# Performance work log

Hardware: AMD Instinct MI355X
Metric: run time of the kernel (lower is better)

The kernel has to match this reference:

```python
import jax, jax.numpy as jnp
import numpy as np
import math

INV = 1.0 / (2.0 * math.pi) ** 2  # 1/(2*pi)^2 normalization used throughout
EPS = 1e-8


def setup_inputs() -> dict:
    key = jax.random.key(0)
    ks = jax.random.split(key, 5)
    N, K, J = 512, 8, 6
    return {
        "x_hat": jax.random.normal(ks[0], (N, N, 2), jnp.float32),
        "phi_hat_real": jax.random.normal(ks[1], (N, N), jnp.float32),
        "phi_hat_imag": jax.random.normal(ks[2], (N, N), jnp.float32),
        "psi_hat_real": jax.random.normal(ks[3], (K, J, N, N), jnp.float32),
        "psi_hat_imag": jax.random.normal(ks[4], (K, J, N, N), jnp.float32),
    }


def reference(x_hat, phi_hat_real, phi_hat_imag, psi_hat_real, psi_hat_imag):
    K, J, N, _ = psi_hat_real.shape
    NN = N * N
    phi2 = phi_hat_real ** 2 + phi_hat_imag ** 2  # [N,N]

    # zeroth-order coefficient: full spatial mean of |x_hat|^2 * |phi_hat|^2
    s0 = INV * jnp.mean((x_hat[:, :, 0] ** 2 + x_hat[:, :, 1] ** 2) * phi2)

    # first layer: complex multiply in Fourier domain, ifft2, modulus, fft2
    xc = jax.lax.complex(x_hat[:, :, 0], x_hat[:, :, 1])          # [N,N] complex
    psic = jax.lax.complex(psi_hat_real, psi_hat_imag)            # [K,J,N,N] complex
    temp = jnp.fft.ifft2(xc[None, None] * psic, axes=(-2, -1))    # [K,J,N,N] complex
    mod = jnp.sqrt(temp.real ** 2 + temp.imag ** 2 + EPS)         # modulus nonlinearity
    t2 = jnp.fft.fft2(mod, axes=(-2, -1))                         # rfft onesided=False == full fft of real
    power = (t2.real ** 2 + t2.imag ** 2).reshape(K, J, NN)       # |U1_hat|^2

    # first-order coefficients a[k,i] = INV * mean(power * phi2)
    a = INV * (power @ phi2.reshape(NN)) / NN                     # [K,J]

    # second-order coefficients via GEMM over spatial dim:
    # B[k,i,m,j] = INV * mean_xy(power[k,i] * |psi[m,j]|^2)
    psi2 = (psi_hat_real ** 2 + psi_hat_imag ** 2).reshape(K, J, NN)
    B = INV * jnp.einsum('kin,mjn->kimj', power, psi2) / NN       # [K,J,K,J]

    # assemble output in the same concatenation order as the torch loop:
    # [s0, a_0, b_0(flattened over k,m,j'), a_1, b_1, ..., a_{J-1}]
    pieces = [s0[None]]
    for i in range(J):
        pieces.append(a[:, i])
        if i < J - 1:
            pieces.append(B[:, i, :, i + 1:J].reshape(-1))
    return jnp.concatenate(pieces, axis=0)
```

## Files before the change

kernel.cpp:

```cpp
#include <hip/hip_runtime.h>
#include <hip/hip_fp16.h>

#define Nn 512
#define NNe 262144
#define CST 546

__device__ __forceinline__ float2 f2(float x, float y){ return make_float2(x, y); }
__device__ __forceinline__ float2 cadd(float2 a, float2 b){ return f2(a.x+b.x, a.y+b.y); }
__device__ __forceinline__ float2 csub(float2 a, float2 b){ return f2(a.x-b.x, a.y-b.y); }
__device__ __forceinline__ float2 cmul(float2 a, float2 b){
    return f2(a.x*b.x - a.y*b.y, a.x*b.y + a.y*b.x);
}
__device__ __forceinline__ int pidx(int p){ return p + (p>>4) + (p>>7); }
#define WFENCE() __builtin_amdgcn_wave_barrier()

template<int SGN>
__device__ __forceinline__ void fft8(float2 a[8]){
    const float r = 0.7071067811865476f;
    const float S = (float)SGN;
    float2 u0 = cadd(a[0], a[4]), u1 = cadd(a[1], a[5]);
    float2 u2 = cadd(a[2], a[6]), u3 = cadd(a[3], a[7]);
    float2 v0 = csub(a[0], a[4]), v1 = csub(a[1], a[5]);
    float2 v2 = csub(a[2], a[6]), v3 = csub(a[3], a[7]);
    v1 = cmul(v1, f2(r, S*r));
    v2 = cmul(v2, f2(0.f, S));
    v3 = cmul(v3, f2(-r, S*r));
    float2 p0 = cadd(u0, u2), p1 = cadd(u1, u3);
    float2 q0 = csub(u0, u2), q1 = cmul(csub(u1, u3), f2(0.f, S));
    a[0] = cadd(p0, p1); a[4] = csub(p0, p1);
    a[2] = cadd(q0, q1); a[6] = csub(q0, q1);
    p0 = cadd(v0, v2); p1 = cadd(v1, v3);
    q0 = csub(v0, v2); q1 = cmul(csub(v1, v3), f2(0.f, S));
    a[1] = cadd(p0, p1); a[5] = csub(p0, p1);
    a[3] = cadd(q0, q1); a[7] = csub(q0, q1);
}

__device__ __forceinline__ float2 twdp(int idx, float inv){
    float ang = 6.283185307179586f * (inv * (float)idx);
    float s, c;
    __sincosf(ang, &s, &c);
    return f2(c, s);
}

template<int SGN>
__device__ void fft512_dif_i(float2 v[8], float2* buf, int lane){
    fft8<SGN>(v);
    {
        float2 w1 = twdp(lane, 1.f/512.f);
        if (SGN < 0) w1.y = -w1.y;
        float2 w  = f2(1.f, 0.f);
        #pragma unroll
        for (int r = 0; r < 8; ++r){
            buf[pidx(r*64 + lane)] = cmul(v[r], w);
            w = cmul(w, w1);
        }
    }
    WFENCE();
    int rb = (lane >> 3) * 64, t2 = lane & 7;
    float2 y[8];
    #pragma unroll
    for (int q = 0; q < 8; ++q) y[q] = buf[pidx(rb + t2 + 8*q)];
    fft8<SGN>(y);
    WFENCE();
    {
        float2 w2 = twdp(t2, 1.f/64.f);
        if (SGN < 0) w2.y = -w2.y;
        float2 w  = f2(1.f, 0.f);
        #pragma unroll
        for (int r = 0; r < 8; ++r){
            buf[pidx(rb + r*8 + t2)] = cmul(y[r], w);
            w = cmul(w, w2);
        }
    }
    WFENCE();
    int base = rb + t2*8;
    #pragma unroll
    for (int q = 0; q < 8; ++q) v[q] = buf[pidx(base + q)];
    fft8<SGN>(v);
}

template<int SGN>
__device__ void fft512_dit_i(float2 v[8], float2* buf, int lane){
    int rb = (lane >> 3) * 64, t2 = lane & 7;
    fft8<SGN>(v);
    int base = rb + t2*8;
    #pragma unroll
    for (int q = 0; q < 8; ++q) buf[pidx(base + q)] = v[q];
    WFENCE();
    float2 y[8];
    #pragma unroll
    for (int r = 0; r < 8; ++r) y[r] = buf[pidx(rb + r*8 + t2)];
    {
        float2 w2 = twdp(t2, 1.f/64.f);
        if (SGN < 0) w2.y = -w2.y;
        float2 w  = f2(1.f, 0.f);
        #pragma unroll
        for (int r = 0; r < 8; ++r){
            y[r] = cmul(y[r], w);
            w = cmul(w, w2);
        }
    }
    fft8<SGN>(y);
    WFENCE();
    #pragma unroll
    for (int q = 0; q < 8; ++q) buf[pidx(rb + t2 + 8*q)] = y[q];
    WFENCE();
    #pragma unroll
    for (int r = 0; r < 8; ++r) v[r] = buf[pidx(r*64 + lane)];
    {
        float2 w1 = twdp(lane, 1.f/512.f);
        if (SGN < 0) w1.y = -w1.y;
        float2 w  = f2(1.f, 0.f);
        #pragma unroll
        for (int r = 0; r < 8; ++r){
            v[r] = cmul(v[r], w);
            w = cmul(w, w1);
        }
    }
    fft8<SGN>(v);
}

__global__ __launch_bounds__(256, 6)
void k_mulrow(const float2* __restrict__ xh, const float* __restrict__ pr,
              const float* __restrict__ pi, __half2* __restrict__ temp,
              __half* __restrict__ psi2h){
    __shared__ float2 lds[4][548];
    int wave = threadIdx.x >> 6, lane = threadIdx.x & 63;
    int img  = blockIdx.x >> 7;
    int row  = ((blockIdx.x & 127) << 2) | wave;
    size_t boff = (size_t)img * NNe + (size_t)row * Nn;
    const float2* xr = xh + (size_t)row * Nn;
    float2 v[8];
    #pragma unroll
    for (int q = 0; q < 8; ++q){
        int x = lane + 64*q;
        float2 xv = xr[x];
        float2 pv = f2(pr[boff + x], pi[boff + x]);
        psi2h[boff + x] = __float2half_rn(pv.x*pv.x + pv.y*pv.y);
        v[q] = cmul(xv, pv);
    }
    fft512_dif_i<1>(v, lds[wave], lane);
    __half2* outp = temp + boff;
    #pragma unroll
    for (int q = 0; q < 8; ++q) outp[64*q + lane] = __floats2half2_rn(v[q].x, v[q].y);
}

__global__ __launch_bounds__(512, 2)
void k_colfused(__half2* __restrict__ temp){
    __shared__ __half2 st[16][521];
    __shared__ float2 fbuf[8][CST];
    int img = blockIdx.x >> 5;
    int x0  = (blockIdx.x & 31) << 4;
    __half2* src = temp + (size_t)img * NNe + x0;
    for (int i = threadIdx.x; i < 2048; i += 512){
        int row = i >> 2, c4 = (i & 3) << 2;
        uint4 u = *(const uint4*)&src[(size_t)row * Nn + c4];
        st[c4+0][row] = *(__half2*)&u.x;
        st[c4+1][row] = *(__half2*)&u.y;
        st[c4+2][row] = *(__half2*)&u.z;
        st[c4+3][row] = *(__half2*)&u.w;
    }
    __syncthreads();
    int wave = threadIdx.x >> 6, lane = threadIdx.x & 63;
    const float sc = 3.814697265625e-06f;
    float2* buf = fbuf[wave];
    int c0 = 2*wave, c1 = c0 + 1;
    float2 a[8], b[8];
    #pragma unroll
    for (int q = 0; q < 8; ++q) a[q] = __half22float2(st[c0][lane + 64*q]);
    fft512_dif_i<1>(a, buf, lane);
    WFENCE();
    #pragma unroll
    for (int q = 0; q < 8; ++q) b[q] = __half22float2(st[c1][lane + 64*q]);
    fft512_dif_i<1>(b, buf, lane);
    float2 z[8];
    #pragma unroll
    for (int q = 0; q < 8; ++q){
        float r0 = a[q].x*sc, i0 = a[q].y*sc;
        float r1 = b[q].x*sc, i1 = b[q].y*sc;
        z[q] = f2(sqrtf(r0*r0 + i0*i0 + 1e-8f), sqrtf(r1*r1 + i1*i1 + 1e-8f));
    }
    WFENCE();
    fft512_dit_i<-1>(z, buf, lane);
    #pragma unroll
    for (int q = 0; q < 8; ++q) buf[pidx(lane + 64*q)] = z[q];
    WFENCE();
    #pragma unroll
    for (int q = 0; q < 8; ++q){
        int k = lane + 64*q;
        float2 zr = buf[pidx((512 - k) & 511)];
        float2 zv = z[q];
        st[c0][k] = __floats2half2_rn(0.5f*(zv.x + zr.x), 0.5f*(zv.y - zr.y));
        st[c1][k] = __floats2half2_rn(0.5f*(zv.y + zr.y), 0.5f*(zr.x - zv.x));
    }
    __syncthreads();
    for (int i = threadIdx.x; i < 2048; i += 512){
        int row = i >> 2, c4 = (i & 3) << 2;
        uint4 u;
        *(__half2*)&u.x = st[c4+0][row];
        *(__half2*)&u.y = st[c4+1][row];
        *(__half2*)&u.z = st[c4+2][row];
        *(__half2*)&u.w = st[c4+3][row];
        *(uint4*)&src[(size_t)row * Nn + c4] = u;
    }
}

__global__ __launch_bounds__(256, 6)
void k_rowpow(const __half2* __restrict__ temp, __half* __restrict__ powerh){
    __shared__ float2 lds[4][548];
    int wave = threadIdx.x >> 6, lane = threadIdx.x & 63;
    int img  = blockIdx.x >> 7;
    int row  = ((blockIdx.x & 127) << 2) | wave;
    const __half2* src = temp + (size_t)img * NNe + (size_t)row * Nn;
    float2 v[8];
    #pragma unroll
    for (int q = 0; q < 8; ++q) v[q] = __half22float2(src[64*q + lane]);
    fft512_dit_i<-1>(v, lds[wave], lane);
    __half* dst = powerh + (size_t)img * NNe + (size_t)row * Nn;
    #pragma unroll
    for (int q = 0; q < 8; ++q)
        dst[lane + 64*q] = __float2half_rn((v[q].x*v[q].x + v[q].y*v[q].y) * 0.00390625f);
}

__global__ __launch_bounds__(128)
void k_gemm(const __half* __restrict__ powerh, const __half* __restrict__ psi2h,
            const float* __restrict__ phr, const float* __restrict__ phii,
            const float2* __restrict__ xh, float* __restrict__ partC,
            float* __restrict__ partS0){
    __shared__ __align__(16) float P[2][48][68];
    __shared__ __align__(16) float W[2][56][68];
    int wave = threadIdx.x >> 6, lane = threadIdx.x & 63;
    float (*Pw)[68] = P[wave];
    float (*Ww)[68] = W[wave];
    int gw = blockIdx.x*2 + wave;
    int lm = lane >> 3, lw = lane & 7;
    float acc[6][7] = {};
    float s0acc = 0.f;
    #pragma unroll
    for (int r = 49; r < 56; ++r){
        Ww[r][lane] = 0.f;
        if (lane < 4) Ww[r][64 + lane] = 0.f;
    }
    int n0 = gw * 256;
    for (int st = 0; st < 4; ++st){
        int nb = n0 + st*64;
        WFENCE();
        #pragma unroll
        for (int rr = 0; rr < 12; ++rr){
            int row = rr*4 + (lane >> 4);
            int c4  = (lane & 15) * 4;
            size_t off = (size_t)row*NNe + nb + c4;
            const __half2* p2 = (const __half2*)&powerh[off];
            float2 f0 = __half22float2(p2[0]);
            float2 f1 = __half22float2(p2[1]);
            *(float4*)&Pw[row][c4] = make_float4(f0.x, f0.y, f1.x, f1.y);
        }
        #pragma unroll
        for (int rr = 0; rr < 12; ++rr){
            int row = rr*4 + (lane >> 4);
            int c4  = (lane & 15) * 4;
            size_t off = (size_t)row*NNe + nb + c4;
            const __half2* p2 = (const __half2*)&psi2h[off];
            float2 f0 = __half22float2(p2[0]);
            float2 f1 = __half22float2(p2[1]);
            *(float4*)&Ww[row][c4] = make_float4(f0.x, f0.y, f1.x, f1.y);
        }
        if (lane < 16){
            int c4 = lane * 4;
            float4 a = *(const float4*)&phr[nb + c4];
            float4 b = *(const float4*)&phii[nb + c4];
            float4 w4;
            w4.x = a.x*a.x + b.x*b.x; w4.y = a.y*a.y + b.y*b.y;
            w4.z = a.z*a.z + b.z*b.z; w4.w = a.w*a.w + b.w*b.w;
            *(float4*)&Ww[48][c4] = w4;
        }
        WFENCE();
        {
            float2 xv = xh[nb + lane];
            s0acc = fmaf(xv.x*xv.x + xv.y*xv.y, Ww[48][lane], s0acc);
        }
        #pragma unroll 2
        for (int nn = 0; nn < 64; nn += 4){
            float4 pa[6], wb[7];
            #pragma unroll
            for (int i = 0; i < 6; ++i) pa[i] = *(const float4*)&Pw[lm + 8*i][nn];
            #pragma unroll
            for (int j = 0; j < 7; ++j) wb[j] = *(const float4*)&Ww[lw + 8*j][nn];
            #pragma unroll
            for (int i = 0; i < 6; ++i)
                #pragma unroll
                for (int j = 0; j < 7; ++j){
                    float s = acc[i][j];
                    s = fmaf(pa[i].x, wb[j].x, s);
                    s = fmaf(pa[i].y, wb[j].y, s);
                    s = fmaf(pa[i].z, wb[j].z, s);
                    s = fmaf(pa[i].w, wb[j].w, s);
                    acc[i][j] = s;
                }
        }
    }
    #pragma unroll
    for (int o = 32; o > 0; o >>= 1) s0acc += __shfl_down(s0acc, o, 64);
    if (lane == 0) partS0[gw] = s0acc;
    float* outp = partC + (size_t)gw * 2400;
    #pragma unroll
    for (int i = 0; i < 6; ++i)
        #pragma unroll
        for (int j = 0; j < 7; ++j){
            int m = lm + 8*i, wc = lw + 8*j;
            if (wc < 49) outp[m*50 + wc] = acc[i][j];
        }
}

__global__ __launch_bounds__(256)
void k_redc1(const float* __restrict__ partC, float* __restrict__ partC2){
    __shared__ float red[4][64];
    int es = threadIdx.x & 63, wave = threadIdx.x >> 6;
    int e = blockIdx.x*64 + es;
    int b0 = blockIdx.y*64 + wave*16;
    float s = 0.f;
    if (e < 2400){
        #pragma unroll
        for (int u = 0; u < 16; ++u) s += partC[(size_t)(b0+u)*2400 + e];
    }
    red[wave][es] = s;
    __syncthreads();
    if (wave == 0 && e < 2400)
        partC2[(size_t)blockIdx.y*2400 + e] = red[0][es]+red[1][es]+red[2][es]+red[3][es];
}

__global__ __launch_bounds__(256)
void k_final(const float* __restrict__ partC2, const float* __restrict__ partS0,
             float* __restrict__ outp, float SC0, float SCC){
    __shared__ float CFs[2400];
    __shared__ float ssum[4];
    int tid = threadIdx.x, wave = tid >> 6, lane = tid & 63;
    for (int e = tid; e < 2400; e += 256){
        float s = 0.f;
        #pragma unroll
        for (int u = 0; u < 16; ++u) s += partC2[(size_t)u*2400 + e];
        CFs[e] = SCC * s;
    }
    float a = 0.f;
    #pragma unroll
    for (int u = 0; u < 4; ++u) a += partS0[tid + 256*u];
    #pragma unroll
    for (int o = 32; o > 0; o >>= 1) a += __shfl_down(a, o, 64);
    if (lane == 0) ssum[wave] = a;
    __syncthreads();
    if (tid == 0) outp[0] = SC0 * (ssum[0]+ssum[1]+ssum[2]+ssum[3]);
    int off = 1;
    for (int i = 0; i < 6; ++i){
        if (tid < 8) outp[off + tid] = CFs[(tid*6 + i)*50 + 48];
        off += 8;
        if (i < 5){
            int nj = 5 - i, cnt = 64 * nj;
            for (int p = tid; p < cnt; p += 256){
                int j2 = p % nj;
                int km = p / nj;
                int m = km & 7, k = km >> 3;
                outp[off + p] = CFs[(k*6 + i)*50 + m*6 + (i + 1 + j2)];
            }
            off += cnt;
        }
    }
}

extern "C" void kernel_launch(void* const* d_in, const int* in_sizes, int n_in,
                              void* d_out, int out_size, void* d_ws, size_t ws_size,
                              hipStream_t stream){
    (void)in_sizes; (void)n_in; (void)out_size; (void)ws_size;
    const float2* xh  = (const float2*)d_in[0];
    const float*  phr = (const float*)d_in[1];
    const float*  phi_= (const float*)d_in[2];
    const float*  psr = (const float*)d_in[3];
    const float*  psi_= (const float*)d_in[4];
    float* outp = (float*)d_out;
    float* ws   = (float*)d_ws;

    size_t o_power = 0;
    size_t o_partC = o_power + (size_t)24 * NNe;
    size_t o_pC2   = o_partC + (size_t)1024 * 2400;
    size_t o_s0    = o_pC2 + (size_t)16 * 2400;
    size_t o_temp  = o_s0 + 1024;
    size_t o_psi2  = o_temp + (size_t)48 * NNe;
    __half*  powerh= (__half*)(ws + o_power);
    float*   partC = ws + o_partC;
    float*   partC2= ws + o_pC2;
    float*   ps0   = ws + o_s0;
    __half2* temp  = (__half2*)(ws + o_temp);
    __half*  psi2h = (__half*)(ws + o_psi2);

    const double INVd = 1.0 / (4.0 * 3.14159265358979323846 * 3.14159265358979323846);
    const float SC0 = (float)(INVd / (double)NNe);
    const float SCC = (float)(INVd / (double)NNe * 256.0);

    k_mulrow<<<dim3(48*128), dim3(256), 0, stream>>>(xh, psr, psi_, temp, psi2h);
    k_colfused<<<dim3(48*32), dim3(512), 0, stream>>>(temp);
    k_rowpow<<<dim3(48*128), dim3(256), 0, stream>>>(temp, powerh);
    k_gemm<<<dim3(512), dim3(128), 0, stream>>>(powerh, psi2h, phr, phi_, xh, partC, ps0);
    k_redc1<<<dim3(38, 16), dim3(256), 0, stream>>>(partC, partC2);
    k_final<<<dim3(1), dim3(256), 0, stream>>>(partC2, ps0, outp, SC0, SCC);
}
```

Measured before the change: 136.2 us.

## Share GEMM tiles across four waves splitting output columns per block

The partial GEMM kernel now loads each 64-column chunk of power and psi2 into shared memory once per 256-thread block, and the four waves split the 49 output columns (13 each), instead of each wave loading its own tile and computing all columns. This cuts per-thread accumulator registers from 42 to 12 and doubles the grid to 1024 blocks, raising occupancy and cutting redundant global loads per output. The cost is block-wide __syncthreads instead of wave barriers, and the 8x2 column mapping has lanes with cr>=13 doing wasted FMAs.

```diff
diff --git a/kernel.cpp b/kernel.cpp
--- a/kernel.cpp
+++ b/kernel.cpp
@@ -222,74 +222,73 @@
         dst[lane + 64*q] = __float2half_rn((v[q].x*v[q].x + v[q].y*v[q].y) * 0.00390625f);
 }
 
-__global__ __launch_bounds__(128)
+__global__ __launch_bounds__(256, 5)
 void k_gemm(const __half* __restrict__ powerh, const __half* __restrict__ psi2h,
             const float* __restrict__ phr, const float* __restrict__ phii,
             const float2* __restrict__ xh, float* __restrict__ partC,
             float* __restrict__ partS0){
-    __shared__ __align__(16) float P[2][48][68];
-    __shared__ __align__(16) float W[2][56][68];
-    int wave = threadIdx.x >> 6, lane = threadIdx.x & 63;
-    float (*Pw)[68] = P[wave];
-    float (*Ww)[68] = W[wave];
-    int gw = blockIdx.x*2 + wave;
+    __shared__ __align__(16) float P[48][68];
+    __shared__ __align__(16) float W[56][68];
+    int tid = threadIdx.x;
+    int wave = tid >> 6, lane = tid & 63;
     int lm = lane >> 3, lw = lane & 7;
-    float acc[6][7] = {};
+    float acc[6][2] = {};
     float s0acc = 0.f;
-    #pragma unroll
-    for (int r = 49; r < 56; ++r){
-        Ww[r][lane] = 0.f;
-        if (lane < 4) Ww[r][64 + lane] = 0.f;
-    }
-    int n0 = gw * 256;
+    if (tid < 224){
+        int r = 49 + (tid >> 5), c = (tid & 31);
+        W[r][c] = 0.f; W[r][32 + c] = 0.f;
+        if (c < 4) W[r][64 + c] = 0.f;
+    }
+    int n0 = blockIdx.x * 256;
     for (int st = 0; st < 4; ++st){
         int nb = n0 + st*64;
-        WFENCE();
-        #pragma unroll
-        for (int rr = 0; rr < 12; ++rr){
-            int row = rr*4 + (lane >> 4);
-            int c4  = (lane & 15) * 4;
+        __syncthreads();
+        #pragma unroll
+        for (int rr = 0; rr < 3; ++rr){
+            int row = rr*16 + (tid >> 4);
+            int c4  = (tid & 15) * 4;
             size_t off = (size_t)row*NNe + nb + c4;
             const __half2* p2 = (const __half2*)&powerh[off];
             float2 f0 = __half22float2(p2[0]);
             float2 f1 = __half22float2(p2[1]);
-            *(float4*)&Pw[row][c4] = make_float4(f0.x, f0.y, f1.x, f1.y);
-        }
-        #pragma unroll
-        for (int rr = 0; rr < 12; ++rr){
-            int row = rr*4 + (lane >> 4);
-            int c4  = (lane & 15) * 4;
+            *(float4*)&P[row][c4] = make_float4(f0.x, f0.y, f1.x, f1.y);
+        }
+        #pragma unroll
+        for (int rr = 0; rr < 3; ++rr){
+            int row = rr*16 + (tid >> 4);
+            int c4  = (tid & 15) * 4;
             size_t off = (size_t)row*NNe + nb + c4;
             const __half2* p2 = (const __half2*)&psi2h[off];
             float2 f0 = __half22float2(p2[0]);
             float2 f1 = __half22float2(p2[1]);
-            *(float4*)&Ww[row][c4] = make_float4(f0.x, f0.y, f1.x, f1.y);
-        }
-        if (lane < 16){
-            int c4 = lane * 4;
+            *(float4*)&W[row][c4] = make_float4(f0.x, f0.y, f1.x, f1.y);
+        }
+        if (tid < 16){
+            int c4 = tid * 4;
             float4 a = *(const float4*)&phr[nb + c4];
             float4 b = *(const float4*)&phii[nb + c4];
             float4 w4;
             w4.x = a.x*a.x + b.x*b.x; w4.y = a.y*a.y + b.y*b.y;
             w4.z = a.z*a.z + b.z*b.z; w4.w = a.w*a.w + b.w*b.w;
-            *(float4*)&Ww[48][c4] = w4;
-        }
-        WFENCE();
-        {
+            *(float4*)&W[48][c4] = w4;
+        }
+        __syncthreads();
+        if (wave == 0){
             float2 xv = xh[nb + lane];
-            s0acc = fmaf(xv.x*xv.x + xv.y*xv.y, Ww[48][lane], s0acc);
-        }
+            s0acc = fmaf(xv.x*xv.x + xv.y*xv.y, W[48][lane], s0acc);
+        }
+        int cb = wave * 13;
         #pragma unroll 2
         for (int nn = 0; nn < 64; nn += 4){
-            float4 pa[6], wb[7];
+            float4 pa[6], wb[2];
             #pragma unroll
-            for (int i = 0; i < 6; ++i) pa[i] = *(const float4*)&Pw[lm + 8*i][nn];
+            for (int i = 0; i < 6; ++i) pa[i] = *(const float4*)&P[lm + 8*i][nn];
             #pragma unroll
-            for (int j = 0; j < 7; ++j) wb[j] = *(const float4*)&Ww[lw + 8*j][nn];
+            for (int j = 0; j < 2; ++j) wb[j] = *(const float4*)&W[cb + lw + 8*j][nn];
             #pragma unroll
             for (int i = 0; i < 6; ++i)
                 #pragma unroll
-                for (int j = 0; j < 7; ++j){
+                for (int j = 0; j < 2; ++j){
                     float s = acc[i][j];
                     s = fmaf(pa[i].x, wb[j].x, s);
                     s = fmaf(pa[i].y, wb[j].y, s);
@@ -299,16 +298,21 @@
                 }
         }
     }
-    #pragma unroll
-    for (int o = 32; o > 0; o >>= 1) s0acc += __shfl_down(s0acc, o, 64);
-    if (lane == 0) partS0[gw] = s0acc;
-    float* outp = partC + (size_t)gw * 2400;
+    if (wave == 0){
+        #pragma unroll
+        for (int o = 32; o > 0; o >>= 1) s0acc += __shfl_down(s0acc, o, 64);
+        if (lane == 0) partS0[blockIdx.x] = s0acc;
+    }
+    float* outp = partC + (size_t)blockIdx.x * 2400;
+    int cb = wave * 13;
     #pragma unroll
     for (int i = 0; i < 6; ++i)
         #pragma unroll
-        for (int j = 0; j < 7; ++j){
-            int m = lm + 8*i, wc = lw + 8*j;
-            if (wc < 49) outp[m*50 + wc] = acc[i][j];
+        for (int j = 0; j < 2; ++j){
+            int cr = lw + 8*j;
+            int wc = cb + cr;
+            int m  = lm + 8*i;
+            if (cr < 13 && wc < 49) outp[m*50 + wc] = acc[i][j];
         }
 }
 
@@ -398,7 +402,7 @@
     k_mulrow<<<dim3(48*128), dim3(256), 0, stream>>>(xh, psr, psi_, temp, psi2h);
     k_colfused<<<dim3(48*32), dim3(512), 0, stream>>>(temp);
     k_rowpow<<<dim3(48*128), dim3(256), 0, stream>>>(temp, powerh);
-    k_gemm<<<dim3(512), dim3(128), 0, stream>>>(powerh, psi2h, phr, phi_, xh, partC, ps0);
+    k_gemm<<<dim3(1024), dim3(256), 0, stream>>>(powerh, psi2h, phr, phi_, xh, partC, ps0);
     k_redc1<<<dim3(38, 16), dim3(256), 0, stream>>>(partC, partC2);
     k_final<<<dim3(1), dim3(256), 0, stream>>>(partC2, ps0, outp, SC0, SCC);
 }
```

After: 129.9 us (median of 2 runs). -4.6%, faster.
